# Optimization experiments

Measured on AMD Instinct MI355X. Metric: run time of the kernel, lower is better.

## Reference

```python
import jax, jax.numpy as jnp
import numpy as np
import math

NUM_HEADS = 16
D_MODEL = 1024
BATCH = 1
SEQ_LEN = 4096


def alibi_slopes(num_heads):
    # slopes m_h = (256 ** (1/H)) ** -(h+1)
    x = (2.0 ** 8) ** (1.0 / num_heads)
    return jnp.asarray([1.0 / x ** (i + 1) for i in range(num_heads)], dtype=jnp.float32)


def setup_inputs() -> dict:
    key = jax.random.key(0)
    k1, k2 = jax.random.split(key)
    x = jax.random.normal(k1, (BATCH, SEQ_LEN, D_MODEL), dtype=jnp.float32)
    # nn.Linear(d_model, 3*d_model, bias=False); store as [d_model, 3*d_model] so y = x @ w
    w_kqv = jax.random.normal(k2, (D_MODEL, 3 * D_MODEL), dtype=jnp.float32) * (1.0 / math.sqrt(D_MODEL))
    return {"x": x, "w_kqv": w_kqv}


def reference(x, w_kqv):
    B, S, D = x.shape
    H = NUM_HEADS
    dh = D // H
    scale = jnp.asarray(math.sqrt(D), dtype=x.dtype)  # module divides by sqrt(d_model)

    kqv = x @ w_kqv  # [B, S, 3D]
    # NOTE: original chunks as (key, query, value) in that order
    k, q, v = jnp.split(kqv, 3, axis=-1)
    q = q.reshape(B, S, H, dh)
    k = k.reshape(B, S, H, dh)
    v = v.reshape(B, S, H, dh)

    # ALiBi bias: m_h * (j - i), shape [H, S, S]
    pos = jnp.arange(S)
    rel = pos[None, :] - pos[:, None]  # [S, S], x - y
    slopes = alibi_slopes(H).astype(x.dtype)  # [H]
    bias = slopes[:, None, None] * rel.astype(x.dtype)  # [H, S, S]

    score = jnp.einsum('bihd,bjhd->bhij', q, k) / scale + bias[None]  # [B, H, S, S]
    causal = rel <= 0  # j <= i (lower triangular)
    score = jnp.where(causal[None, None], score, jnp.asarray(-jnp.inf, dtype=score.dtype))

    attn = jax.nn.softmax(score, axis=-1)
    out = jnp.einsum('bhij,bjhd->bihd', attn, v).reshape(B, S, D)
    return out
```

## Files before the change

kernel.cpp:

```cpp
#include <hip/hip_runtime.h>
#include <stdint.h>
#include <math.h>

#define SEQ 4096
#define DM  1024
#define NH  16
#define DH  64
#define LOG2E 1.44269504088896341f

typedef short bf16x8 __attribute__((ext_vector_type(8)));
typedef short bf16x4 __attribute__((ext_vector_type(4)));
typedef float f32x4  __attribute__((ext_vector_type(4)));
typedef uint32_t u32x4 __attribute__((ext_vector_type(4)));

typedef const __attribute__((address_space(1))) short* gptr_t;
typedef __attribute__((address_space(3))) short* lptr_t;

__device__ __forceinline__ short f2bf(float f) {
    union { float f; uint32_t u; } x; x.f = f;
    uint32_t r = (x.u + 0x7fffu + ((x.u >> 16) & 1u)) >> 16;
    return (short)r;
}
__device__ __forceinline__ uint32_t pkbf(float lo, float hi) {
    union { float f; uint32_t u; } a, b; a.f = lo; b.f = hi;
    return (a.u >> 16) | (b.u & 0xffff0000u);
}

__device__ __forceinline__ void load_lds16(const short* g, const short* l) {
    __builtin_amdgcn_global_load_lds((gptr_t)(uintptr_t)g,
                                     (lptr_t)(uint32_t)(uintptr_t)l, 16, 0, 0);
}

__device__ __forceinline__ void wgbar() {
    asm volatile("" ::: "memory");
    __builtin_amdgcn_s_barrier();
    asm volatile("" ::: "memory");
}
#define WAITVM(n) asm volatile("s_waitcnt vmcnt(" #n ")" ::: "memory")
#define DSR(d, a, o) asm volatile("ds_read_b128 %0, %1 offset:" o : "=v"(d) : "v"(a))

__global__ __launch_bounds__(256) void cvt_fused(const float* __restrict__ x,
                                                 const float* __restrict__ w,
                                                 short* __restrict__ xb,
                                                 short* __restrict__ wtb) {
    __shared__ float T[64][69];
    const int b = blockIdx.x;
    if (b < 2048) {
        const int i = (b * 256 + threadIdx.x) * 8;
        float4 a0 = ((const float4*)(x + i))[0];
        float4 a1 = ((const float4*)(x + i))[1];
        bf16x8 p;
        p[0]=f2bf(a0.x); p[1]=f2bf(a0.y); p[2]=f2bf(a0.z); p[3]=f2bf(a0.w);
        p[4]=f2bf(a1.x); p[5]=f2bf(a1.y); p[6]=f2bf(a1.z); p[7]=f2bf(a1.w);
        *(bf16x8*)(xb + i) = p;
        return;
    }
    const int bb = b - 2048;
    const int n0 = (bb % 48) * 64, k0 = (bb / 48) * 64;
    const int t = threadIdx.x;
    {
        const int kr = t >> 4, nc = (t & 15) * 4;
        #pragma unroll
        for (int i = 0; i < 4; ++i) {
            float4 v = *(const float4*)(w + (size_t)(k0 + kr + i * 16) * 3072 + n0 + nc);
            T[kr + i * 16][nc + 0] = v.x; T[kr + i * 16][nc + 1] = v.y;
            T[kr + i * 16][nc + 2] = v.z; T[kr + i * 16][nc + 3] = v.w;
        }
    }
    __syncthreads();
    const int nr = t >> 4, kc = (t & 15) * 4;
    #pragma unroll
    for (int i = 0; i < 4; ++i) {
        const int n = n0 + nr + i * 16;
        const float sc = (n >= 1024 && n < 2048) ? (LOG2E / 32.0f) : 1.0f;
        short4 o;
        o.x = f2bf(T[kc + 0][nr + i * 16] * sc);
        o.y = f2bf(T[kc + 1][nr + i * 16] * sc);
        o.z = f2bf(T[kc + 2][nr + i * 16] * sc);
        o.w = f2bf(T[kc + 3][nr + i * 16] * sc);
        *(short4*)(wtb + (size_t)n * 1024 + k0 + kc) = o;
    }
}

__global__ __launch_bounds__(256, 2) void qkv_gemm(const short* __restrict__ xb,
                                                   const short* __restrict__ wtb,
                                                   short* __restrict__ kq,
                                                   short* __restrict__ vt) {
    __shared__ short As[2][8192];
    __shared__ short Bs[2][8192];
    const int col0 = blockIdx.y * 128, row0 = blockIdx.x * 128;
    const int tid = threadIdx.x, w = tid >> 6, lane = tid & 63;
    const int lmod = lane & 15, ldiv = lane >> 4;
    const int wr = (w >> 1) * 64, wc = (w & 1) * 64;

    const int srow = w * 32 + (lane >> 3);
    const int slc  = (lane & 7) ^ ((lane >> 3) & 7);
    const short* gA = xb  + (size_t)(row0 + srow) * 1024 + slc * 8;
    const short* gB = wtb + (size_t)(col0 + srow) * 1024 + slc * 8;
    short* lA = &As[0][0] + w * 2048;
    short* lB = &Bs[0][0] + w * 2048;

    const uint32_t asb = (uint32_t)(uintptr_t)&As[0][0];
    const uint32_t bsb = (uint32_t)(uintptr_t)&Bs[0][0];
    const int xorm = lmod & 7;
    const int rdA = (wr + lmod) * 128 + ((ldiv ^ xorm) << 4);
    const int rdB = (wc + lmod) * 128 + ((ldiv ^ xorm) << 4);

    f32x4 acc[4][4] = {};

    auto stage = [&](int kt, int p) {
        const short* ga = gA + kt * 64;
        const short* gb = gB + kt * 64;
        short* la = lA + p * 8192;
        short* lb = lB + p * 8192;
        #pragma unroll
        for (int q = 0; q < 4; ++q) {
            load_lds16(ga + q * 8192, la + q * 512);
            load_lds16(gb + q * 8192, lb + q * 512);
        }
    };

    stage(0, 0);
    stage(1, 1);
    WAITVM(8);
    wgbar();

    for (int t = 0; t < 16; ++t) {
        const int poff = (t & 1) << 14;
        const int aA0 = (int)asb + poff + rdA, aA1 = aA0 ^ 64;
        const int bA0 = (int)bsb + poff + rdB, bA1 = bA0 ^ 64;
        bf16x8 a0[4], a1[4], b0[4], b1[4];
        DSR(a0[0], aA0, "0");    DSR(a0[1], aA0, "2048");
        DSR(a0[2], aA0, "4096"); DSR(a0[3], aA0, "6144");
        DSR(b0[0], bA0, "0");    DSR(b0[1], bA0, "2048");
        DSR(b0[2], bA0, "4096"); DSR(b0[3], bA0, "6144");
        DSR(a1[0], aA1, "0");    DSR(a1[1], aA1, "2048");
        DSR(a1[2], aA1, "4096"); DSR(a1[3], aA1, "6144");
        DSR(b1[0], bA1, "0");    DSR(b1[1], bA1, "2048");
        DSR(b1[2], bA1, "4096"); DSR(b1[3], bA1, "6144");
        asm volatile("s_waitcnt lgkmcnt(8)" ::: "memory");
        __builtin_amdgcn_sched_barrier(0);
        #pragma unroll
        for (int i = 0; i < 4; ++i)
            #pragma unroll
            for (int j = 0; j < 4; ++j)
                acc[i][j] = __builtin_amdgcn_mfma_f32_16x16x32_bf16(a0[i], b0[j], acc[i][j], 0, 0, 0);
        asm volatile("s_waitcnt lgkmcnt(0)" ::: "memory");
        __builtin_amdgcn_sched_barrier(0);
        #pragma unroll
        for (int i = 0; i < 4; ++i)
            #pragma unroll
            for (int j = 0; j < 4; ++j)
                acc[i][j] = __builtin_amdgcn_mfma_f32_16x16x32_bf16(a1[i], b1[j], acc[i][j], 0, 0, 0);

        wgbar();
        if (t + 2 < 16) {
            stage(t + 2, t & 1);
            WAITVM(8);
            wgbar();
        } else if (t + 1 < 16) {
            WAITVM(0);
            wgbar();
        }
    }

    if (col0 < 2048) {
        #pragma unroll
        for (int i = 0; i < 4; ++i)
            #pragma unroll
            for (int j = 0; j < 4; ++j)
                #pragma unroll
                for (int r = 0; r < 4; ++r)
                    kq[(size_t)(row0 + wr + i * 16 + ldiv * 4 + r) * 2048
                       + col0 + wc + j * 16 + lmod] = f2bf(acc[i][j][r]);
    } else {
        #pragma unroll
        for (int i = 0; i < 4; ++i) {
            const int ig = row0 + wr + i * 16 + ldiv * 4;
            const int kk = ig & 63;
            const int kkp = (kk & 32) | ((kk & 12) << 1) | ((kk & 16) >> 2);
            const int igp = (ig & ~63) | kkp;
            #pragma unroll
            for (int j = 0; j < 4; ++j) {
                const int cg = col0 + wc + j * 16 + lmod - 2048;
                const int h = cg >> 6, d = cg & 63;
                bf16x4 p;
                p[0]=f2bf(acc[i][j][0]); p[1]=f2bf(acc[i][j][1]);
                p[2]=f2bf(acc[i][j][2]); p[3]=f2bf(acc[i][j][3]);
                *(bf16x4*)(vt + (size_t)(h * 64 + d) * SEQ + igp) = p;
            }
        }
    }
}

__global__ __launch_bounds__(256, 4) void attn(const short* __restrict__ kq,
                                               const short* __restrict__ vt,
                                               float* __restrict__ o0,
                                               float* __restrict__ o1,
                                               float* __restrict__ ls0,
                                               float* __restrict__ ls1) {
    __shared__ short Ks[64 * 64];
    __shared__ short Vs[64 * 64];

    const int b = blockIdx.x;
    const int band = b >> 8, pos = b & 255, g = pos >> 5;
    const int qt = (band & 1) ? (24 - band * 8 + g) : (31 - band * 8 - g);
    const int h = (pos >> 1) & 15, s = pos & 1;

    const int tid = threadIdx.x, w = tid >> 6, lane = tid & 63;
    const int lmod = lane & 15, ldiv = lane >> 4;
    const float slope2 = exp2f(-0.5f * (float)(h + 1)) * LOG2E;

    const int sr0 = w * 16 + (lane >> 3), sr1 = sr0 + 8;
    const int sc0 = (lane & 7) ^ (sr0 & 7), sc1 = (lane & 7) ^ (sr1 & 7);

    const int xorm = lmod & 7;
    const int cxs0 = (ldiv ^ xorm) * 8;
    const int cxs1 = ((4 + ldiv) ^ xorm) * 8;

    const int rowbase = qt * 128 + w * 32;

    bf16x8 qf[2][2];
    #pragma unroll
    for (int m = 0; m < 2; ++m) {
        const short* qp = kq + (size_t)(rowbase + m * 16 + lmod) * 2048 + 1024 + h * 64;
        qf[m][0] = *(const bf16x8*)(qp + ldiv * 8);
        qf[m][1] = *(const bf16x8*)(qp + 32 + ldiv * 8);
    }
    int db2[2];
    float pre[2][4];
    #pragma unroll
    for (int m = 0; m < 2; ++m) {
        db2[m] = 4 * ldiv - (rowbase + m * 16 + lmod);
        #pragma unroll
        for (int r = 0; r < 4; ++r) pre[m][r] = slope2 * (float)(db2[m] + r);
    }

    f32x4 O[2][4] = {};
    float lsum[2] = {};
    const int kt0 = s ? (qt + 1) : 0;
    const int kt1 = s ? (2 * qt + 2) : (qt + 1);

    for (int kt = kt0; kt < kt1; ++kt) {
        __syncthreads();
        {
            const short* kb = kq + (size_t)(kt * 64) * 2048 + h * 64;
            load_lds16(kb + (size_t)sr0 * 2048 + sc0 * 8, Ks + (w * 16) * 64);
            load_lds16(kb + (size_t)sr1 * 2048 + sc1 * 8, Ks + (w * 16 + 8) * 64);
            const short* vb = vt + (size_t)(h * 64) * SEQ + kt * 64;
            load_lds16(vb + (size_t)sr0 * SEQ + sc0 * 8, Vs + (w * 16) * 64);
            load_lds16(vb + (size_t)sr1 * SEQ + sc1 * 8, Vs + (w * 16 + 8) * 64);
        }
        __syncthreads();

        const bool diag = (kt >= 2 * qt);
        const int dt = kt * 64;
        const float cb = slope2 * (float)dt;

        #pragma unroll
        for (int ks = 0; ks < 2; ++ks) {
            u32x4 pk0, pk1;
            #pragma unroll
            for (int j1 = 0; j1 < 2; ++j1) {
                const int nt = ks * 2 + j1;
                const float cn = cb + slope2 * (float)(nt * 16);
                f32x4 s0, s1;
                #pragma unroll
                for (int r = 0; r < 4; ++r) { s0[r] = pre[0][r] + cn; s1[r] = pre[1][r] + cn; }
                const short* krow = Ks + (nt * 16 + lmod) * 64;
                const bf16x8 kf0 = *(const bf16x8*)(krow + cxs0);
                const bf16x8 kf1 = *(const bf16x8*)(krow + cxs1);
                s0 = __builtin_amdgcn_mfma_f32_16x16x32_bf16(kf0, qf[0][0], s0, 0, 0, 0);
                s0 = __builtin_amdgcn_mfma_f32_16x16x32_bf16(kf1, qf[0][1], s0, 0, 0, 0);
                s1 = __builtin_amdgcn_mfma_f32_16x16x32_bf16(kf0, qf[1][0], s1, 0, 0, 0);
                s1 = __builtin_amdgcn_mfma_f32_16x16x32_bf16(kf1, qf[1][1], s1, 0, 0, 0);

                float p0[4], p1[4];
                if (diag) {
                    #pragma unroll
                    for (int r = 0; r < 4; ++r) {
                        float v0 = s0[r], v1 = s1[r];
                        if (dt + nt * 16 + r + db2[0] > 0) v0 = -1e30f;
                        if (dt + nt * 16 + r + db2[1] > 0) v1 = -1e30f;
                        p0[r] = __builtin_amdgcn_exp2f(v0);
                        p1[r] = __builtin_amdgcn_exp2f(v1);
                    }
                } else {
                    #pragma unroll
                    for (int r = 0; r < 4; ++r) {
                        p0[r] = __builtin_amdgcn_exp2f(s0[r]);
                        p1[r] = __builtin_amdgcn_exp2f(s1[r]);
                    }
                }
                lsum[0] += (p0[0] + p0[1]) + (p0[2] + p0[3]);
                lsum[1] += (p1[0] + p1[1]) + (p1[2] + p1[3]);
                pk0[j1 * 2]     = pkbf(p0[0], p0[1]);
                pk0[j1 * 2 + 1] = pkbf(p0[2], p0[3]);
                pk1[j1 * 2]     = pkbf(p1[0], p1[1]);
                pk1[j1 * 2 + 1] = pkbf(p1[2], p1[3]);
            }
            const bf16x8 pa0 = __builtin_bit_cast(bf16x8, pk0);
            const bf16x8 pa1 = __builtin_bit_cast(bf16x8, pk1);
            const int cxo = ks ? cxs1 : cxs0;
            #pragma unroll
            for (int nt2 = 0; nt2 < 4; ++nt2) {
                const bf16x8 vf = *(const bf16x8*)(Vs + (nt2 * 16 + lmod) * 64 + cxo);
                O[0][nt2] = __builtin_amdgcn_mfma_f32_16x16x32_bf16(pa0, vf, O[0][nt2], 0, 0, 0);
                O[1][nt2] = __builtin_amdgcn_mfma_f32_16x16x32_bf16(pa1, vf, O[1][nt2], 0, 0, 0);
            }
        }
    }

    #pragma unroll
    for (int m = 0; m < 2; ++m) {
        float v = lsum[m];
        v += __shfl_xor(v, 16);
        v += __shfl_xor(v, 32);
        lsum[m] = v;
    }

    float* ob = s ? o1 : o0;
    float* lb = s ? ls1 : ls0;
    #pragma unroll
    for (int m = 0; m < 2; ++m) {
        const int i0 = rowbase + m * 16 + ldiv * 4;
        #pragma unroll
        for (int nt2 = 0; nt2 < 4; ++nt2)
            #pragma unroll
            for (int r = 0; r < 4; ++r)
                ob[(size_t)(i0 + r) * DM + h * 64 + nt2 * 16 + lmod] = O[m][nt2][r];
    }
    if (ldiv == 0) {
        #pragma unroll
        for (int m = 0; m < 2; ++m)
            lb[h * SEQ + rowbase + m * 16 + lmod] = lsum[m];
    }
}

__global__ __launch_bounds__(256) void combine(float* __restrict__ out,
                                               const float* __restrict__ opart,
                                               const float* __restrict__ ls0,
                                               const float* __restrict__ ls1) {
    const int i8 = (blockIdx.x * 256 + threadIdx.x) * 8;
    const int row = i8 >> 10, col = i8 & 1023, h = col >> 6;
    const float l = ls0[h * SEQ + row] + ls1[h * SEQ + row];
    const float rc = 1.0f / l;
    float4 a0 = *(const float4*)(out + i8);
    float4 a1 = *(const float4*)(out + i8 + 4);
    float4 b0 = *(const float4*)(opart + i8);
    float4 b1 = *(const float4*)(opart + i8 + 4);
    float4 c0, c1;
    c0.x = (a0.x + b0.x) * rc; c0.y = (a0.y + b0.y) * rc;
    c0.z = (a0.z + b0.z) * rc; c0.w = (a0.w + b0.w) * rc;
    c1.x = (a1.x + b1.x) * rc; c1.y = (a1.y + b1.y) * rc;
    c1.z = (a1.z + b1.z) * rc; c1.w = (a1.w + b1.w) * rc;
    *(float4*)(out + i8) = c0;
    *(float4*)(out + i8 + 4) = c1;
}

extern "C" void kernel_launch(void* const* d_in, const int* in_sizes, int n_in,
                              void* d_out, int out_size, void* d_ws, size_t ws_size,
                              hipStream_t stream) {
    const float* x = (const float*)d_in[0];
    const float* w = (const float*)d_in[1];
    float* out = (float*)d_out;

    char* ws = (char*)d_ws;
    short* kq    = (short*)(ws);
    short* vt    = (short*)(ws + ((size_t)16 << 20));
    short* xb    = (short*)(ws + ((size_t)24 << 20));
    short* wtb   = (short*)(ws + ((size_t)32 << 20));
    float* opart = (float*)(ws + ((size_t)24 << 20));
    float* ls0   = (float*)(ws + ((size_t)40 << 20));
    float* ls1   = (float*)(ws + ((size_t)40 << 20) + (256 << 10));

    cvt_fused<<<2048 + 768, 256, 0, stream>>>(x, w, xb, wtb);
    qkv_gemm <<<dim3(SEQ / 128, 3072 / 128), 256, 0, stream>>>(xb, wtb, kq, vt);
    attn     <<<1024, 256, 0, stream>>>(kq, vt, out, opart, ls0, ls1);
    combine  <<<SEQ * DM / (256 * 8), 256, 0, stream>>>(out, opart, ls0, ls1);
}
```

Measured before the change: 160.3 us.

## Double-buffer K/V tiles in attention and issue explicit LDS reads ahead of MFMAs

The attention kernel now keeps two LDS buffers each for K and V. It prefetches the tile for step t+2 with global_load_lds while the current tile is computed, replacing the old load-then-sync loop. K and V fragments are read with inline ds_read_b128 and explicit lgkmcnt waits, so V reads for the PV product are issued while the QK MFMAs and softmax run. The bf16 pack helper is also changed to a single v_perm instruction. LDS use doubles per block, which may reduce occupancy under the 4-blocks launch bound, and the manual waitcnt and barrier bookkeeping adds risk.

```diff
diff --git a/kernel.cpp b/kernel.cpp
--- a/kernel.cpp
+++ b/kernel.cpp
@@ -23,7 +23,7 @@
 }
 __device__ __forceinline__ uint32_t pkbf(float lo, float hi) {
     union { float f; uint32_t u; } a, b; a.f = lo; b.f = hi;
-    return (a.u >> 16) | (b.u & 0xffff0000u);
+    return __builtin_amdgcn_perm(b.u, a.u, 0x07060302u);
 }
 
 __device__ __forceinline__ void load_lds16(const short* g, const short* l) {
@@ -37,6 +37,8 @@
     asm volatile("" ::: "memory");
 }
 #define WAITVM(n) asm volatile("s_waitcnt vmcnt(" #n ")" ::: "memory")
+#define WAITLGKM(n) do { asm volatile("s_waitcnt lgkmcnt(" #n ")" ::: "memory"); \
+                         __builtin_amdgcn_sched_barrier(0); } while (0)
 #define DSR(d, a, o) asm volatile("ds_read_b128 %0, %1 offset:" o : "=v"(d) : "v"(a))
 
 __global__ __launch_bounds__(256) void cvt_fused(const float* __restrict__ x,
@@ -138,15 +140,13 @@
         DSR(a1[2], aA1, "4096"); DSR(a1[3], aA1, "6144");
         DSR(b1[0], bA1, "0");    DSR(b1[1], bA1, "2048");
         DSR(b1[2], bA1, "4096"); DSR(b1[3], bA1, "6144");
-        asm volatile("s_waitcnt lgkmcnt(8)" ::: "memory");
-        __builtin_amdgcn_sched_barrier(0);
+        WAITLGKM(8);
         #pragma unroll
         for (int i = 0; i < 4; ++i)
             #pragma unroll
             for (int j = 0; j < 4; ++j)
                 acc[i][j] = __builtin_amdgcn_mfma_f32_16x16x32_bf16(a0[i], b0[j], acc[i][j], 0, 0, 0);
-        asm volatile("s_waitcnt lgkmcnt(0)" ::: "memory");
-        __builtin_amdgcn_sched_barrier(0);
+        WAITLGKM(0);
         #pragma unroll
         for (int i = 0; i < 4; ++i)
             #pragma unroll
@@ -199,8 +199,8 @@
                                                float* __restrict__ o1,
                                                float* __restrict__ ls0,
                                                float* __restrict__ ls1) {
-    __shared__ short Ks[64 * 64];
-    __shared__ short Vs[64 * 64];
+    __shared__ short Ks[2][4096];
+    __shared__ short Vs[2][4096];
 
     const int b = blockIdx.x;
     const int band = b >> 8, pos = b & 255, g = pos >> 5;
@@ -215,8 +215,9 @@
     const int sc0 = (lane & 7) ^ (sr0 & 7), sc1 = (lane & 7) ^ (sr1 & 7);
 
     const int xorm = lmod & 7;
-    const int cxs0 = (ldiv ^ xorm) * 8;
-    const int cxs1 = ((4 + ldiv) ^ xorm) * 8;
+    const uint32_t ksb = (uint32_t)(uintptr_t)&Ks[0][0];
+    const uint32_t vsb = (uint32_t)(uintptr_t)&Vs[0][0];
+    const int rdO = lmod * 128 + (((ldiv ^ xorm)) << 4);
 
     const int rowbase = qt * 128 + w * 32;
 
@@ -240,46 +241,63 @@
     float lsum[2] = {};
     const int kt0 = s ? (qt + 1) : 0;
     const int kt1 = s ? (2 * qt + 2) : (qt + 1);
-
-    for (int kt = kt0; kt < kt1; ++kt) {
-        __syncthreads();
-        {
-            const short* kb = kq + (size_t)(kt * 64) * 2048 + h * 64;
-            load_lds16(kb + (size_t)sr0 * 2048 + sc0 * 8, Ks + (w * 16) * 64);
-            load_lds16(kb + (size_t)sr1 * 2048 + sc1 * 8, Ks + (w * 16 + 8) * 64);
-            const short* vb = vt + (size_t)(h * 64) * SEQ + kt * 64;
-            load_lds16(vb + (size_t)sr0 * SEQ + sc0 * 8, Vs + (w * 16) * 64);
-            load_lds16(vb + (size_t)sr1 * SEQ + sc1 * 8, Vs + (w * 16 + 8) * 64);
-        }
-        __syncthreads();
-
+    const int n = kt1 - kt0;
+
+    auto stage = [&](int kt_, int p) {
+        const short* kb = kq + (size_t)(kt_ * 64) * 2048 + h * 64;
+        load_lds16(kb + (size_t)sr0 * 2048 + sc0 * 8, &Ks[p][(w * 16) * 64]);
+        load_lds16(kb + (size_t)sr1 * 2048 + sc1 * 8, &Ks[p][(w * 16 + 8) * 64]);
+        const short* vb = vt + (size_t)(h * 64) * SEQ + kt_ * 64;
+        load_lds16(vb + (size_t)sr0 * SEQ + sc0 * 8, &Vs[p][(w * 16) * 64]);
+        load_lds16(vb + (size_t)sr1 * SEQ + sc1 * 8, &Vs[p][(w * 16 + 8) * 64]);
+    };
+
+    stage(kt0, 0);
+    if (n > 1) { stage(kt0 + 1, 1); WAITVM(4); } else { WAITVM(0); }
+    wgbar();
+
+    for (int t = 0; t < n; ++t) {
+        const int kt = kt0 + t;
+        const int boff = (t & 1) << 13;
+        const int aK = (int)ksb + boff + rdO;
+        const int aV = (int)vsb + boff + rdO;
         const bool diag = (kt >= 2 * qt);
         const int dt = kt * 64;
         const float cb = slope2 * (float)dt;
 
         #pragma unroll
         for (int ks = 0; ks < 2; ++ks) {
+            const int aKs = aK + ks * 4096;
+            const int aKx = aKs ^ 64;
+            const int aVs = ks ? (aV ^ 64) : aV;
+            bf16x8 kA[2], kB[2], vf[4];
+            DSR(kA[0], aKs, "0");    DSR(kB[0], aKx, "0");
+            DSR(kA[1], aKs, "2048"); DSR(kB[1], aKx, "2048");
+            WAITLGKM(0);
+
+            f32x4 sj[2][2];
+            #pragma unroll
+            for (int j1 = 0; j1 < 2; ++j1) {
+                const float cn = cb + slope2 * (float)((ks * 2 + j1) * 16);
+                #pragma unroll
+                for (int r = 0; r < 4; ++r) { sj[j1][0][r] = pre[0][r] + cn; sj[j1][1][r] = pre[1][r] + cn; }
+                sj[j1][0] = __builtin_amdgcn_mfma_f32_16x16x32_bf16(kA[j1], qf[0][0], sj[j1][0], 0, 0, 0);
+                sj[j1][0] = __builtin_amdgcn_mfma_f32_16x16x32_bf16(kB[j1], qf[0][1], sj[j1][0], 0, 0, 0);
+                sj[j1][1] = __builtin_amdgcn_mfma_f32_16x16x32_bf16(kA[j1], qf[1][0], sj[j1][1], 0, 0, 0);
+                sj[j1][1] = __builtin_amdgcn_mfma_f32_16x16x32_bf16(kB[j1], qf[1][1], sj[j1][1], 0, 0, 0);
+            }
+            DSR(vf[0], aVs, "0");    DSR(vf[1], aVs, "2048");
+            DSR(vf[2], aVs, "4096"); DSR(vf[3], aVs, "6144");
+
             u32x4 pk0, pk1;
             #pragma unroll
             for (int j1 = 0; j1 < 2; ++j1) {
                 const int nt = ks * 2 + j1;
-                const float cn = cb + slope2 * (float)(nt * 16);
-                f32x4 s0, s1;
-                #pragma unroll
-                for (int r = 0; r < 4; ++r) { s0[r] = pre[0][r] + cn; s1[r] = pre[1][r] + cn; }
-                const short* krow = Ks + (nt * 16 + lmod) * 64;
-                const bf16x8 kf0 = *(const bf16x8*)(krow + cxs0);
-                const bf16x8 kf1 = *(const bf16x8*)(krow + cxs1);
-                s0 = __builtin_amdgcn_mfma_f32_16x16x32_bf16(kf0, qf[0][0], s0, 0, 0, 0);
-                s0 = __builtin_amdgcn_mfma_f32_16x16x32_bf16(kf1, qf[0][1], s0, 0, 0, 0);
-                s1 = __builtin_amdgcn_mfma_f32_16x16x32_bf16(kf0, qf[1][0], s1, 0, 0, 0);
-                s1 = __builtin_amdgcn_mfma_f32_16x16x32_bf16(kf1, qf[1][1], s1, 0, 0, 0);
-
                 float p0[4], p1[4];
                 if (diag) {
                     #pragma unroll
                     for (int r = 0; r < 4; ++r) {
-                        float v0 = s0[r], v1 = s1[r];
+                        float v0 = sj[j1][0][r], v1 = sj[j1][1][r];
                         if (dt + nt * 16 + r + db2[0] > 0) v0 = -1e30f;
                         if (dt + nt * 16 + r + db2[1] > 0) v1 = -1e30f;
                         p0[r] = __builtin_amdgcn_exp2f(v0);
@@ -288,8 +306,8 @@
                 } else {
                     #pragma unroll
                     for (int r = 0; r < 4; ++r) {
-                        p0[r] = __builtin_amdgcn_exp2f(s0[r]);
-                        p1[r] = __builtin_amdgcn_exp2f(s1[r]);
+                        p0[r] = __builtin_amdgcn_exp2f(sj[j1][0][r]);
+                        p1[r] = __builtin_amdgcn_exp2f(sj[j1][1][r]);
                     }
                 }
                 lsum[0] += (p0[0] + p0[1]) + (p0[2] + p0[3]);
@@ -301,13 +319,22 @@
             }
             const bf16x8 pa0 = __builtin_bit_cast(bf16x8, pk0);
             const bf16x8 pa1 = __builtin_bit_cast(bf16x8, pk1);
-            const int cxo = ks ? cxs1 : cxs0;
+            WAITLGKM(0);
             #pragma unroll
             for (int nt2 = 0; nt2 < 4; ++nt2) {
-                const bf16x8 vf = *(const bf16x8*)(Vs + (nt2 * 16 + lmod) * 64 + cxo);
-                O[0][nt2] = __builtin_amdgcn_mfma_f32_16x16x32_bf16(pa0, vf, O[0][nt2], 0, 0, 0);
-                O[1][nt2] = __builtin_amdgcn_mfma_f32_16x16x32_bf16(pa1, vf, O[1][nt2], 0, 0, 0);
+                O[0][nt2] = __builtin_amdgcn_mfma_f32_16x16x32_bf16(pa0, vf[nt2], O[0][nt2], 0, 0, 0);
+                O[1][nt2] = __builtin_amdgcn_mfma_f32_16x16x32_bf16(pa1, vf[nt2], O[1][nt2], 0, 0, 0);
             }
+        }
+
+        wgbar();
+        if (t + 2 < n) {
+            stage(kt0 + t + 2, t & 1);
+            WAITVM(4);
+            wgbar();
+        } else if (t + 1 < n) {
+            WAITVM(0);
+            wgbar();
         }
     }
 
```

New measurement: 197.5 us. +23.2%, slower.

## Fuse split-KV combine into attention via atomic last-block-finishes pattern

Applied to the files above, without the earlier changes.

Drops the separate combine kernel. Each attention block writes its partial output and row sums, then atomically bumps a per-(query tile, head) counter, and the second finisher merges both partials and normalizes directly into the output. This removes one kernel launch and a full extra pass over the output and partial buffers. In exchange it adds threadfences, an atomic per block, and a flag reset folded into the conversion kernel. The last finisher still reloads its partner's partial from memory.

```diff
diff --git a/kernel.cpp b/kernel.cpp
--- a/kernel.cpp
+++ b/kernel.cpp
@@ -37,14 +37,21 @@
     asm volatile("" ::: "memory");
 }
 #define WAITVM(n) asm volatile("s_waitcnt vmcnt(" #n ")" ::: "memory")
+#define WAITLGKM(n) do { asm volatile("s_waitcnt lgkmcnt(" #n ")" ::: "memory"); \
+                         __builtin_amdgcn_sched_barrier(0); } while (0)
 #define DSR(d, a, o) asm volatile("ds_read_b128 %0, %1 offset:" o : "=v"(d) : "v"(a))
 
 __global__ __launch_bounds__(256) void cvt_fused(const float* __restrict__ x,
                                                  const float* __restrict__ w,
                                                  short* __restrict__ xb,
-                                                 short* __restrict__ wtb) {
+                                                 short* __restrict__ wtb,
+                                                 int* __restrict__ flags) {
     __shared__ float T[64][69];
     const int b = blockIdx.x;
+    if (b == 0) {
+        flags[threadIdx.x] = 0;
+        flags[256 + threadIdx.x] = 0;
+    }
     if (b < 2048) {
         const int i = (b * 256 + threadIdx.x) * 8;
         float4 a0 = ((const float4*)(x + i))[0];
@@ -138,15 +145,13 @@
         DSR(a1[2], aA1, "4096"); DSR(a1[3], aA1, "6144");
         DSR(b1[0], bA1, "0");    DSR(b1[1], bA1, "2048");
         DSR(b1[2], bA1, "4096"); DSR(b1[3], bA1, "6144");
-        asm volatile("s_waitcnt lgkmcnt(8)" ::: "memory");
-        __builtin_amdgcn_sched_barrier(0);
+        WAITLGKM(8);
         #pragma unroll
         for (int i = 0; i < 4; ++i)
             #pragma unroll
             for (int j = 0; j < 4; ++j)
                 acc[i][j] = __builtin_amdgcn_mfma_f32_16x16x32_bf16(a0[i], b0[j], acc[i][j], 0, 0, 0);
-        asm volatile("s_waitcnt lgkmcnt(0)" ::: "memory");
-        __builtin_amdgcn_sched_barrier(0);
+        WAITLGKM(0);
         #pragma unroll
         for (int i = 0; i < 4; ++i)
             #pragma unroll
@@ -198,7 +203,8 @@
                                                float* __restrict__ o0,
                                                float* __restrict__ o1,
                                                float* __restrict__ ls0,
-                                               float* __restrict__ ls1) {
+                                               float* __restrict__ ls1,
+                                               int* __restrict__ flags) {
     __shared__ short Ks[64 * 64];
     __shared__ short Vs[64 * 64];
 
@@ -335,27 +341,33 @@
         for (int m = 0; m < 2; ++m)
             lb[h * SEQ + rowbase + m * 16 + lmod] = lsum[m];
     }
-}
-
-__global__ __launch_bounds__(256) void combine(float* __restrict__ out,
-                                               const float* __restrict__ opart,
-                                               const float* __restrict__ ls0,
-                                               const float* __restrict__ ls1) {
-    const int i8 = (blockIdx.x * 256 + threadIdx.x) * 8;
-    const int row = i8 >> 10, col = i8 & 1023, h = col >> 6;
-    const float l = ls0[h * SEQ + row] + ls1[h * SEQ + row];
-    const float rc = 1.0f / l;
-    float4 a0 = *(const float4*)(out + i8);
-    float4 a1 = *(const float4*)(out + i8 + 4);
-    float4 b0 = *(const float4*)(opart + i8);
-    float4 b1 = *(const float4*)(opart + i8 + 4);
-    float4 c0, c1;
-    c0.x = (a0.x + b0.x) * rc; c0.y = (a0.y + b0.y) * rc;
-    c0.z = (a0.z + b0.z) * rc; c0.w = (a0.w + b0.w) * rc;
-    c1.x = (a1.x + b1.x) * rc; c1.y = (a1.y + b1.y) * rc;
-    c1.z = (a1.z + b1.z) * rc; c1.w = (a1.w + b1.w) * rc;
-    *(float4*)(out + i8) = c0;
-    *(float4*)(out + i8 + 4) = c1;
+
+    __threadfence();
+    __syncthreads();
+    __shared__ int finsh;
+    if (tid == 0) finsh = atomicAdd(&flags[qt * NH + h], 1);
+    __syncthreads();
+    if (finsh == 0) return;
+    __threadfence();
+
+    const float* pb  = s ? o0 : o1;
+    const float* plb = s ? ls0 : ls1;
+    const float* olb = s ? ls1 : ls0;
+    #pragma unroll
+    for (int m = 0; m < 2; ++m) {
+        const int i0 = rowbase + m * 16 + ldiv * 4;
+        float rc[4];
+        #pragma unroll
+        for (int r = 0; r < 4; ++r)
+            rc[r] = 1.0f / (olb[h * SEQ + i0 + r] + plb[h * SEQ + i0 + r]);
+        #pragma unroll
+        for (int nt2 = 0; nt2 < 4; ++nt2)
+            #pragma unroll
+            for (int r = 0; r < 4; ++r) {
+                const size_t idx = (size_t)(i0 + r) * DM + h * 64 + nt2 * 16 + lmod;
+                o0[idx] = (O[m][nt2][r] + pb[idx]) * rc[r];
+            }
+    }
 }
 
 extern "C" void kernel_launch(void* const* d_in, const int* in_sizes, int n_in,
@@ -373,9 +385,9 @@
     float* opart = (float*)(ws + ((size_t)24 << 20));
     float* ls0   = (float*)(ws + ((size_t)40 << 20));
     float* ls1   = (float*)(ws + ((size_t)40 << 20) + (256 << 10));
-
-    cvt_fused<<<2048 + 768, 256, 0, stream>>>(x, w, xb, wtb);
+    int*   flags = (int*)  (ws + ((size_t)40 << 20) + (512 << 10));
+
+    cvt_fused<<<2048 + 768, 256, 0, stream>>>(x, w, xb, wtb, flags);
     qkv_gemm <<<dim3(SEQ / 128, 3072 / 128), 256, 0, stream>>>(xb, wtb, kq, vt);
-    attn     <<<1024, 256, 0, stream>>>(kq, vt, out, opart, ls0, ls1);
-    combine  <<<SEQ * DM / (256 * 8), 256, 0, stream>>>(out, opart, ls0, ls1);
-}
+    attn     <<<1024, 256, 0, stream>>>(kq, vt, out, opart, ls0, ls1, flags);
+}
```

Result: slower. 429.7 us (+168.1%).

## Halve attention query tile to 64 rows and double the grid

Applied to the files above, without the earlier changes.

The attention kernel now gives each workgroup a 64-row query tile instead of 128 rows, so each wave handles 16 rows instead of 32. The grid doubles to 2048 blocks and the key range is split in half per block differently. The aim is more parallelism and less per-block register pressure, which could raise occupancy and improve load balance. The cost is that each K/V tile loaded into LDS is reused by half as many query rows, which doubles K/V traffic and barrier overhead per unit of work. A small macro cleanup for the lgkmcnt wait is also included.

```diff
diff --git a/kernel.cpp b/kernel.cpp
--- a/kernel.cpp
+++ b/kernel.cpp
@@ -37,6 +37,8 @@
     asm volatile("" ::: "memory");
 }
 #define WAITVM(n) asm volatile("s_waitcnt vmcnt(" #n ")" ::: "memory")
+#define WAITLGKM(n) do { asm volatile("s_waitcnt lgkmcnt(" #n ")" ::: "memory"); \
+                         __builtin_amdgcn_sched_barrier(0); } while (0)
 #define DSR(d, a, o) asm volatile("ds_read_b128 %0, %1 offset:" o : "=v"(d) : "v"(a))
 
 __global__ __launch_bounds__(256) void cvt_fused(const float* __restrict__ x,
@@ -138,15 +140,13 @@
         DSR(a1[2], aA1, "4096"); DSR(a1[3], aA1, "6144");
         DSR(b1[0], bA1, "0");    DSR(b1[1], bA1, "2048");
         DSR(b1[2], bA1, "4096"); DSR(b1[3], bA1, "6144");
-        asm volatile("s_waitcnt lgkmcnt(8)" ::: "memory");
-        __builtin_amdgcn_sched_barrier(0);
+        WAITLGKM(8);
         #pragma unroll
         for (int i = 0; i < 4; ++i)
             #pragma unroll
             for (int j = 0; j < 4; ++j)
                 acc[i][j] = __builtin_amdgcn_mfma_f32_16x16x32_bf16(a0[i], b0[j], acc[i][j], 0, 0, 0);
-        asm volatile("s_waitcnt lgkmcnt(0)" ::: "memory");
-        __builtin_amdgcn_sched_barrier(0);
+        WAITLGKM(0);
         #pragma unroll
         for (int i = 0; i < 4; ++i)
             #pragma unroll
@@ -204,7 +204,7 @@
 
     const int b = blockIdx.x;
     const int band = b >> 8, pos = b & 255, g = pos >> 5;
-    const int qt = (band & 1) ? (24 - band * 8 + g) : (31 - band * 8 - g);
+    const int j = (band & 1) ? (56 - band * 8 + g) : (63 - band * 8 - g);
     const int h = (pos >> 1) & 15, s = pos & 1;
 
     const int tid = threadIdx.x, w = tid >> 6, lane = tid & 63;
@@ -218,28 +218,24 @@
     const int cxs0 = (ldiv ^ xorm) * 8;
     const int cxs1 = ((4 + ldiv) ^ xorm) * 8;
 
-    const int rowbase = qt * 128 + w * 32;
-
-    bf16x8 qf[2][2];
+    const int rowbase = j * 64 + w * 16;
+
+    bf16x8 qf[2];
+    {
+        const short* qp = kq + (size_t)(rowbase + lmod) * 2048 + 1024 + h * 64;
+        qf[0] = *(const bf16x8*)(qp + ldiv * 8);
+        qf[1] = *(const bf16x8*)(qp + 32 + ldiv * 8);
+    }
+    const int db2 = 4 * ldiv - (rowbase + lmod);
+    float pre[4];
     #pragma unroll
-    for (int m = 0; m < 2; ++m) {
-        const short* qp = kq + (size_t)(rowbase + m * 16 + lmod) * 2048 + 1024 + h * 64;
-        qf[m][0] = *(const bf16x8*)(qp + ldiv * 8);
-        qf[m][1] = *(const bf16x8*)(qp + 32 + ldiv * 8);
-    }
-    int db2[2];
-    float pre[2][4];
-    #pragma unroll
-    for (int m = 0; m < 2; ++m) {
-        db2[m] = 4 * ldiv - (rowbase + m * 16 + lmod);
-        #pragma unroll
-        for (int r = 0; r < 4; ++r) pre[m][r] = slope2 * (float)(db2[m] + r);
-    }
-
-    f32x4 O[2][4] = {};
-    float lsum[2] = {};
-    const int kt0 = s ? (qt + 1) : 0;
-    const int kt1 = s ? (2 * qt + 2) : (qt + 1);
+    for (int r = 0; r < 4; ++r) pre[r] = slope2 * (float)(db2 + r);
+
+    f32x4 O[4] = {};
+    float lsum = 0.0f;
+    const int hh = (j + 2) >> 1;
+    const int kt0 = s ? hh : 0;
+    const int kt1 = s ? (j + 1) : hh;
 
     for (int kt = kt0; kt < kt1; ++kt) {
         __syncthreads();
@@ -253,88 +249,70 @@
         }
         __syncthreads();
 
-        const bool diag = (kt >= 2 * qt);
+        const bool diag = (kt >= j);
         const int dt = kt * 64;
         const float cb = slope2 * (float)dt;
 
         #pragma unroll
         for (int ks = 0; ks < 2; ++ks) {
-            u32x4 pk0, pk1;
+            u32x4 pk;
             #pragma unroll
             for (int j1 = 0; j1 < 2; ++j1) {
                 const int nt = ks * 2 + j1;
                 const float cn = cb + slope2 * (float)(nt * 16);
-                f32x4 s0, s1;
+                f32x4 s0;
                 #pragma unroll
-                for (int r = 0; r < 4; ++r) { s0[r] = pre[0][r] + cn; s1[r] = pre[1][r] + cn; }
+                for (int r = 0; r < 4; ++r) s0[r] = pre[r] + cn;
                 const short* krow = Ks + (nt * 16 + lmod) * 64;
                 const bf16x8 kf0 = *(const bf16x8*)(krow + cxs0);
                 const bf16x8 kf1 = *(const bf16x8*)(krow + cxs1);
-                s0 = __builtin_amdgcn_mfma_f32_16x16x32_bf16(kf0, qf[0][0], s0, 0, 0, 0);
-                s0 = __builtin_amdgcn_mfma_f32_16x16x32_bf16(kf1, qf[0][1], s0, 0, 0, 0);
-                s1 = __builtin_amdgcn_mfma_f32_16x16x32_bf16(kf0, qf[1][0], s1, 0, 0, 0);
-                s1 = __builtin_amdgcn_mfma_f32_16x16x32_bf16(kf1, qf[1][1], s1, 0, 0, 0);
-
-                float p0[4], p1[4];
+                s0 = __builtin_amdgcn_mfma_f32_16x16x32_bf16(kf0, qf[0], s0, 0, 0, 0);
+                s0 = __builtin_amdgcn_mfma_f32_16x16x32_bf16(kf1, qf[1], s0, 0, 0, 0);
+
+                float p0[4];
                 if (diag) {
                     #pragma unroll
                     for (int r = 0; r < 4; ++r) {
-                        float v0 = s0[r], v1 = s1[r];
-                        if (dt + nt * 16 + r + db2[0] > 0) v0 = -1e30f;
-                        if (dt + nt * 16 + r + db2[1] > 0) v1 = -1e30f;
+                        float v0 = s0[r];
+                        if (dt + nt * 16 + r + db2 > 0) v0 = -1e30f;
                         p0[r] = __builtin_amdgcn_exp2f(v0);
-                        p1[r] = __builtin_amdgcn_exp2f(v1);
                     }
                 } else {
                     #pragma unroll
-                    for (int r = 0; r < 4; ++r) {
+                    for (int r = 0; r < 4; ++r)
                         p0[r] = __builtin_amdgcn_exp2f(s0[r]);
-                        p1[r] = __builtin_amdgcn_exp2f(s1[r]);
-                    }
                 }
-                lsum[0] += (p0[0] + p0[1]) + (p0[2] + p0[3]);
-                lsum[1] += (p1[0] + p1[1]) + (p1[2] + p1[3]);
-                pk0[j1 * 2]     = pkbf(p0[0], p0[1]);
-                pk0[j1 * 2 + 1] = pkbf(p0[2], p0[3]);
-                pk1[j1 * 2]     = pkbf(p1[0], p1[1]);
-                pk1[j1 * 2 + 1] = pkbf(p1[2], p1[3]);
+                lsum += (p0[0] + p0[1]) + (p0[2] + p0[3]);
+                pk[j1 * 2]     = pkbf(p0[0], p0[1]);
+                pk[j1 * 2 + 1] = pkbf(p0[2], p0[3]);
             }
-            const bf16x8 pa0 = __builtin_bit_cast(bf16x8, pk0);
-            const bf16x8 pa1 = __builtin_bit_cast(bf16x8, pk1);
+            const bf16x8 pa = __builtin_bit_cast(bf16x8, pk);
             const int cxo = ks ? cxs1 : cxs0;
             #pragma unroll
             for (int nt2 = 0; nt2 < 4; ++nt2) {
                 const bf16x8 vf = *(const bf16x8*)(Vs + (nt2 * 16 + lmod) * 64 + cxo);
-                O[0][nt2] = __builtin_amdgcn_mfma_f32_16x16x32_bf16(pa0, vf, O[0][nt2], 0, 0, 0);
-                O[1][nt2] = __builtin_amdgcn_mfma_f32_16x16x32_bf16(pa1, vf, O[1][nt2], 0, 0, 0);
+                O[nt2] = __builtin_amdgcn_mfma_f32_16x16x32_bf16(pa, vf, O[nt2], 0, 0, 0);
             }
         }
     }
 
-    #pragma unroll
-    for (int m = 0; m < 2; ++m) {
-        float v = lsum[m];
+    {
+        float v = lsum;
         v += __shfl_xor(v, 16);
         v += __shfl_xor(v, 32);
-        lsum[m] = v;
+        lsum = v;
     }
 
     float* ob = s ? o1 : o0;
     float* lb = s ? ls1 : ls0;
+    const int i0 = rowbase + ldiv * 4;
     #pragma unroll
-    for (int m = 0; m < 2; ++m) {
-        const int i0 = rowbase + m * 16 + ldiv * 4;
-        #pragma unroll
-        for (int nt2 = 0; nt2 < 4; ++nt2)
-            #pragma unroll
-            for (int r = 0; r < 4; ++r)
-                ob[(size_t)(i0 + r) * DM + h * 64 + nt2 * 16 + lmod] = O[m][nt2][r];
-    }
-    if (ldiv == 0) {
-        #pragma unroll
-        for (int m = 0; m < 2; ++m)
-            lb[h * SEQ + rowbase + m * 16 + lmod] = lsum[m];
-    }
+    for (int nt2 = 0; nt2 < 4; ++nt2)
+        #pragma unroll
+        for (int r = 0; r < 4; ++r)
+            ob[(size_t)(i0 + r) * DM + h * 64 + nt2 * 16 + lmod] = O[nt2][r];
+    if (ldiv == 0)
+        lb[h * SEQ + rowbase + lmod] = lsum;
 }
 
 __global__ __launch_bounds__(256) void combine(float* __restrict__ out,
@@ -376,6 +354,6 @@
 
     cvt_fused<<<2048 + 768, 256, 0, stream>>>(x, w, xb, wtb);
     qkv_gemm <<<dim3(SEQ / 128, 3072 / 128), 256, 0, stream>>>(xb, wtb, kq, vt);
-    attn     <<<1024, 256, 0, stream>>>(kq, vt, out, opart, ls0, ls1);
+    attn     <<<2048, 256, 0, stream>>>(kq, vt, out, opart, ls0, ls1);
     combine  <<<SEQ * DM / (256 * 8), 256, 0, stream>>>(out, opart, ls0, ls1);
 }
```

After: 161.7 us. About the same (+0.9%).
